# Kernel optimization log

Measured on AMD Instinct MI355X. Metric: run time of the kernel, lower is better.

## Reference

```python
import jax, jax.numpy as jnp
import numpy as np

D = 768      # hidden_dim
H = 12       # num_heads
DH = D // H  # head_dim = 64
L = 12       # num_layers
V = 50257    # vocab_size
M = 16       # mini_batch_size (TTT chunk)
LR = 1.0     # ttt_learning_rate
EPS = 1e-5
ROPE_BASE = 10000.0


def _ln(x, w, b):
    mu = jnp.mean(x, axis=-1, keepdims=True)
    var = jnp.mean((x - mu) ** 2, axis=-1, keepdims=True)
    return (x - mu) / jnp.sqrt(var + EPS) * w + b


def _rope(x):
    # x: (B, H, S, DH)
    S, dh = x.shape[2], x.shape[3]
    half = dh // 2
    freqs = 1.0 / (ROPE_BASE ** (jnp.arange(half, dtype=x.dtype) / half))
    ang = jnp.arange(S, dtype=x.dtype)[:, None] * freqs[None, :]  # (S, half)
    cos, sin = jnp.cos(ang), jnp.sin(ang)
    x1, x2 = x[..., :half], x[..., half:]
    return jnp.concatenate([x1 * cos - x2 * sin, x1 * sin + x2 * cos], axis=-1)


def setup_inputs() -> dict:
    key = jax.random.key(0)
    ks = jax.random.split(key, 12)
    std = 0.02
    B, S = 4, 1024
    inp = {
        "input_ids": jax.random.randint(ks[0], (B, S), 0, V),
        "tok_emb": jax.random.normal(ks[1], (V, D), jnp.float32) * std,
        "emb_ln_w": jnp.ones((D,), jnp.float32),
        "emb_ln_b": jnp.zeros((D,), jnp.float32),
        "wq": jax.random.normal(ks[2], (L, D, D), jnp.float32) * std,
        "wk": jax.random.normal(ks[3], (L, D, D), jnp.float32) * std,
        "wv": jax.random.normal(ks[4], (L, D, D), jnp.float32) * std,
        "wo": jax.random.normal(ks[5], (L, D, D), jnp.float32) * std,
        "n1w": jnp.ones((L, D), jnp.float32),
        "n1b": jnp.zeros((L, D), jnp.float32),
        "n2w": jnp.ones((L, D), jnp.float32),
        "n2b": jnp.zeros((L, D), jnp.float32),
        "m1w": jax.random.normal(ks[6], (L, D, 4 * D), jnp.float32) * std,
        "m1b": jnp.zeros((L, 4 * D), jnp.float32),
        "m2w": jax.random.normal(ks[7], (L, 4 * D, D), jnp.float32) * std,
        "m2b": jnp.zeros((L, D), jnp.float32),
        "onw": jnp.ones((D,), jnp.float32),
        "onb": jnp.zeros((D,), jnp.float32),
    }
    return inp


def _forward(input_ids, tok_emb, emb_ln_w, emb_ln_b, wq, wk, wv, wo,
             n1w, n1b, n2w, n2b, m1w, m1b, m2w, m2b, onw, onb):
    B, S = input_ids.shape
    nc = S // M
    eta = LR / M
    mask = jnp.tril(jnp.ones((M, M), tok_emb.dtype))

    x = tok_emb[input_ids]                      # (B, S, D) token embedding
    x = _ln(x, emb_ln_w, emb_ln_b)

    def layer(x, p):
        (lwq, lwk, lwv, lwo, ln1w, ln1b, ln2w, ln2b,
         lm1w, lm1b, lm2w, lm2b) = p
        h = _ln(x, ln1w, ln1b)

        def proj(w):
            return (h @ w).reshape(B, S, H, DH).transpose(0, 2, 1, 3)  # (B,H,S,DH)

        q, k, v = proj(lwq), proj(lwk), proj(lwv)
        q, k = _rope(q), _rope(k)

        def chunks(t):  # (B,H,S,DH) -> (nc,B,H,M,DH)
            return t.reshape(B, H, nc, M, DH).transpose(2, 0, 1, 3, 4)

        qc, kc, vc = chunks(q), chunks(k), chunks(v)
        W0 = jnp.zeros((B, H, DH, DH), x.dtype)  # fast-weight state per head

        def step(W, c):
            qm, km, vm = c                                   # (B,H,M,DH)
            # reconstruction error of current fast weights on this chunk
            E = jnp.einsum('bhmd,bhde->bhme', km, W) - vm    # (B,H,M,DH)
            # causal intra-chunk correction (dual form of per-token GD)
            A = jnp.einsum('bhmd,bhnd->bhmn', qm, km) * mask
            O = (jnp.einsum('bhmd,bhde->bhme', qm, W)
                 - eta * jnp.einsum('bhmn,bhne->bhme', A, E))
            Wn = W - eta * jnp.einsum('bhmd,bhme->bhde', km, E)
            return Wn, O

        _, O = jax.lax.scan(step, W0, (qc, kc, vc))          # (nc,B,H,M,DH)
        o = O.transpose(1, 2, 0, 3, 4).reshape(B, H, S, DH)
        o = o.transpose(0, 2, 1, 3).reshape(B, S, D)
        x = x + o @ lwo

        h2 = _ln(x, ln2w, ln2b)
        x = x + jax.nn.gelu(h2 @ lm1w + lm1b) @ lm2w + lm2b
        return x, None

    x, _ = jax.lax.scan(layer, x,
                        (wq, wk, wv, wo, n1w, n1b, n2w, n2b,
                         m1w, m1b, m2w, m2b))
    x = _ln(x, onw, onb)
    logits = x @ tok_emb.T                                    # tied LM head
    return logits


def reference(input_ids, tok_emb, emb_ln_w, emb_ln_b, wq, wk, wv, wo,
              n1w, n1b, n2w, n2b, m1w, m1b, m2w, m2b, onw, onb):
    return _forward(input_ids, tok_emb, emb_ln_w, emb_ln_b, wq, wk, wv, wo,
                    n1w, n1b, n2w, n2b, m1w, m1b, m2w, m2b, onw, onb)
```

## Files before the change

### kernel.cpp

```cpp
#include <hip/hip_runtime.h>
#include <cstdint>
#include <cstddef>

#define Dm 768
#define Hh 12
#define DHd 64
#define Ll 12
#define Vv 50257
#define Vp 50304
#define Tt 4096
#define Ff 3072
#define QS 2304
#define ETA (1.0f/16.0f)

typedef __attribute__((ext_vector_type(8))) _Float16 half8;
typedef __attribute__((ext_vector_type(8))) unsigned short ushort8;
typedef __attribute__((ext_vector_type(4))) float f32x4;

static __device__ __forceinline__ unsigned short f2h(float f){
  union { _Float16 h; unsigned short u; } c; c.h = (_Float16)f; return c.u;
}
static __device__ __forceinline__ float h2f(unsigned short u){
  union { unsigned short u; _Float16 h; } c; c.u = u; return (float)c.h;
}
static __device__ __forceinline__ float4 h4(ushort4 u){
  float4 f; f.x=h2f(u.x); f.y=h2f(u.y); f.z=h2f(u.z); f.w=h2f(u.w); return f;
}
static __device__ __forceinline__ void gload16(const void* g, void* l){
  __builtin_amdgcn_global_load_lds((const __attribute__((address_space(1))) unsigned int*)g,
                                   (__attribute__((address_space(3))) unsigned int*)l, 16, 0, 0);
}
static __device__ __forceinline__ size_t pan_off(int ks, size_t M, int row, int k){
  return ((size_t)ks*M + row)*128 + (size_t)(((k*2) ^ ((row & 7) << 4)));
}

__global__ __launch_bounds__(256)
void convwt_kernel(const float* __restrict__ src, unsigned short* __restrict__ dst,
                   int K, int Ns, int Nd, int coff)
{
  const int l  = blockIdx.y;
  const int nb = blockIdx.x % (Ns/64);
  const int ks = blockIdx.x / (Ns/64);
  const int t  = threadIdx.x;
  __shared__ float tile[64][65];
  const float* W = src + (size_t)l*K*Ns;
  {
    const int r = t >> 2, c0 = (t & 3) * 16;
    const float* s = W + (size_t)(ks*64 + r)*Ns + nb*64 + c0;
    #pragma unroll
    for (int i = 0; i < 4; ++i) {
      const float4 f = *(const float4*)(s + i*4);
      tile[r][c0+i*4+0]=f.x; tile[r][c0+i*4+1]=f.y; tile[r][c0+i*4+2]=f.z; tile[r][c0+i*4+3]=f.w;
    }
  }
  __syncthreads();
  const int n   = t >> 2;
  const int kk0 = (t & 3) * 16;
  const int gn  = coff + nb*64 + n;
  unsigned short bh[16];
  #pragma unroll
  for (int i = 0; i < 16; ++i) bh[i] = f2h(tile[kk0 + i][n]);
  const size_t rowb = ((size_t)l*K*Nd + ((size_t)ks*Nd + gn)*64) * 2;
  const int swz = (gn & 7) << 4;
  char* bD = (char*)dst + rowb;
  *(ushort8*)(bD + ((kk0*2)      ^ swz)) = *(ushort8*)&bh[0];
  *(ushort8*)(bD + ((kk0*2 + 16) ^ swz)) = *(ushort8*)&bh[8];
}

__global__ __launch_bounds__(256)
void convtok_kernel(const float* __restrict__ src, unsigned short* __restrict__ dst)
{
  const int total = 12 * Vp * 8;
  for (int gi = blockIdx.x*256 + threadIdx.x; gi < total; gi += gridDim.x*256) {
    const int j  = gi & 7;
    const int v  = (gi >> 3) % Vp;
    const int ks = gi / (8 * Vp);
    ushort8 u;
    if (v < Vv) {
      const float* s = src + (size_t)v*Dm + ks*64 + j*8;
      const float4 f0 = *(const float4*)s, f1 = *(const float4*)(s+4);
      u[0]=f2h(f0.x); u[1]=f2h(f0.y); u[2]=f2h(f0.z); u[3]=f2h(f0.w);
      u[4]=f2h(f1.x); u[5]=f2h(f1.y); u[6]=f2h(f1.z); u[7]=f2h(f1.w);
    } else {
      #pragma unroll
      for (int q = 0; q < 8; ++q) u[q] = 0;
    }
    const size_t rowb = ((size_t)ks*Vp + v) * 128;
    *(ushort8*)((char*)dst + rowb + ((j*16) ^ ((v&7)<<4))) = u;
  }
}

__global__ __launch_bounds__(256)
void rtab_kernel(float* __restrict__ rt)
{
  const int idx = blockIdx.x*256 + threadIdx.x;
  if (idx >= 1024*64) return;
  const int s = idx >> 6, c = idx & 63, d = c & 31;
  const float freq = powf(10000.0f, -(float)d * (1.0f/32.0f));
  const float ang  = (float)s * freq;
  rt[idx] = (c < 32) ? cosf(ang) : sinf(ang);
}

template<int OMODE>
__global__ __launch_bounds__(256)
void ln_kernel(const float* __restrict__ in, const int* __restrict__ ids,
               const float* __restrict__ w, const float* __restrict__ b,
               void* __restrict__ o1)
{
  const int row = blockIdx.x;
  const int t = threadIdx.x;
  const float* px = in + (ids ? (size_t)ids[row] * Dm : (size_t)row * Dm);
  float x0 = px[t], x1 = px[t+256], x2 = px[t+512];
  float s  = x0 + x1 + x2;
  float s2 = x0*x0 + x1*x1 + x2*x2;
  #pragma unroll
  for (int o = 32; o > 0; o >>= 1) { s += __shfl_xor(s, o); s2 += __shfl_xor(s2, o); }
  __shared__ float ls[4], ls2[4];
  if ((t & 63) == 0) { ls[t>>6] = s; ls2[t>>6] = s2; }
  __syncthreads();
  s  = ls[0]+ls[1]+ls[2]+ls[3];
  s2 = ls2[0]+ls2[1]+ls2[2]+ls2[3];
  const float mu  = s * (1.0f/Dm);
  const float var = s2 * (1.0f/Dm) - mu*mu;
  const float rs  = rsqrtf(var + 1e-5f);
  #pragma unroll
  for (int i = 0; i < 3; ++i) {
    const int c = t + i*256;
    const float xv = (i==0) ? x0 : (i==1) ? x1 : x2;
    const float vv_ = (xv-mu)*rs*w[c] + b[c];
    if (OMODE == 0) {
      ((float*)o1)[(size_t)row * Dm + c] = vv_;
    } else {
      *(unsigned short*)((char*)o1 + pan_off(c >> 6, Tt, row, c & 63)) = f2h(vv_);
    }
  }
}

static __device__ __forceinline__ float4 rot4(float4 a, float4 p, float4 rc, float4 rs, bool hi){
  float4 o;
  if (hi) { o.x = p.x*rs.x + a.x*rc.x; o.y = p.y*rs.y + a.y*rc.y;
            o.z = p.z*rs.z + a.z*rc.z; o.w = p.w*rs.w + a.w*rc.w; }
  else    { o.x = a.x*rc.x - p.x*rs.x; o.y = a.y*rc.y - p.y*rs.y;
            o.z = a.z*rc.z - p.z*rs.z; o.w = a.w*rc.w - p.w*rs.w; }
  return o;
}

__global__ __launch_bounds__(256)
void ttt_scan_kernel(const unsigned short* __restrict__ qkv, const float* __restrict__ rt,
                     unsigned short* __restrict__ ob)
{
  const int head = blockIdx.x >> 2;
  const int es   = blockIdx.x & 3;
  const int b  = head / Hh;
  const int hd = head % Hh;
  const int t  = threadIdx.x;
  __shared__ float Wm[16][68];
  __shared__ float kms[16][68];
  __shared__ float qms[16][68];
  __shared__ float EsT[16][20];
  __shared__ float Asc[16][20];

  const int e   = t & 15;
  const int m16 = t >> 4;
  const int sr  = t >> 4;
  const int sc  = (t & 15) * 4;
  const bool hi = (sc >= 32);

  for (int i = t; i < 16*68; i += 256) ((float*)Wm)[i] = 0.0f;

  const int tb0 = b * 1024;
  const size_t gbase = (size_t)hd * DHd;

  float4 krR, qrR;
  {
    const size_t ro = (size_t)(tb0 + sr)*QS + gbase;
    const float4 kr = h4(*(const ushort4*)&qkv[ro + Dm + sc]);
    const float4 kp = h4(*(const ushort4*)&qkv[ro + Dm + (sc^32)]);
    const float4 qr = h4(*(const ushort4*)&qkv[ro + sc]);
    const float4 qp = h4(*(const ushort4*)&qkv[ro + (sc^32)]);
    const float4 rc = *(const float4*)&rt[sr*64 + (sc&31)];
    const float4 rs = *(const float4*)&rt[sr*64 + 32 + (sc&31)];
    krR = rot4(kr, kp, rc, rs, hi);
    qrR = rot4(qr, qp, rc, rs, hi);
  }
  __syncthreads();

  for (int c = 0; c < 64; ++c) {
    const int tb = tb0 + c*16;
    *(float4*)&kms[sr][sc] = krR;
    *(float4*)&qms[sr][sc] = qrR;
    __syncthreads();
    if (c < 63) {
      const size_t ro = (size_t)(tb + 16 + sr)*QS + gbase;
      const float4 kr = h4(*(const ushort4*)&qkv[ro + Dm + sc]);
      const float4 kp = h4(*(const ushort4*)&qkv[ro + Dm + (sc^32)]);
      const float4 qr = h4(*(const ushort4*)&qkv[ro + sc]);
      const float4 qp = h4(*(const ushort4*)&qkv[ro + (sc^32)]);
      const int sN = (c+1)*16 + sr;
      const float4 rc = *(const float4*)&rt[sN*64 + (sc&31)];
      const float4 rs = *(const float4*)&rt[sN*64 + 32 + (sc&31)];
      krR = rot4(kr, kp, rc, rs, hi);
      qrR = rot4(qr, qp, rc, rs, hi);
    }
    const float vreg = h2f(qkv[(size_t)(tb+m16)*QS + 2*Dm + gbase + es*16 + e]);
    float aE = -vreg, aO = 0.0f, aA = 0.0f;
    #pragma unroll
    for (int d4 = 0; d4 < 64; d4 += 4) {
      const float4 wv = *(const float4*)&Wm[e][d4];
      const float4 km = *(const float4*)&kms[m16][d4];
      const float4 qm = *(const float4*)&qms[m16][d4];
      const float4 ke = *(const float4*)&kms[e][d4];
      aE += km.x*wv.x + km.y*wv.y + km.z*wv.z + km.w*wv.w;
      aO += qm.x*wv.x + qm.y*wv.y + qm.z*wv.z + qm.w*wv.w;
      aA += qm.x*ke.x + qm.y*ke.y + qm.z*ke.z + qm.w*ke.w;
    }
    EsT[e][m16] = aE;
    Asc[m16][e] = (e <= m16) ? (-ETA * aA) : 0.0f;
    __syncthreads();
    float esr[16];
    float acc = aO;
    #pragma unroll
    for (int n4 = 0; n4 < 16; n4 += 4) {
      const float4 ev = *(const float4*)&EsT[e][n4];
      const float4 av = *(const float4*)&Asc[m16][n4];
      esr[n4]=ev.x; esr[n4+1]=ev.y; esr[n4+2]=ev.z; esr[n4+3]=ev.w;
      acc += av.x*ev.x + av.y*ev.y + av.z*ev.z + av.w*ev.w;
    }
    *(unsigned short*)((char*)ob + pan_off(hd, Tt, tb + m16, es*16 + e)) = f2h(acc);
    {
      const int d0 = m16 * 4;
      float4 wacc; wacc.x = 0.0f; wacc.y = 0.0f; wacc.z = 0.0f; wacc.w = 0.0f;
      #pragma unroll
      for (int m = 0; m < 16; ++m) {
        const float4 km = *(const float4*)&kms[m][d0];
        const float ev = esr[m];
        wacc.x += km.x*ev; wacc.y += km.y*ev; wacc.z += km.z*ev; wacc.w += km.w*ev;
      }
      float4 wv = *(float4*)&Wm[e][d0];
      wv.x -= ETA*wacc.x; wv.y -= ETA*wacc.y; wv.z -= ETA*wacc.z; wv.w -= ETA*wacc.w;
      *(float4*)&Wm[e][d0] = wv;
    }
    __syncthreads();
  }
}

static __device__ __forceinline__ float gelu_f(float x){
  const float u = 0.7978845608028654f * (x + 0.044715f * x*x*x);
  return 0.5f * x * (1.0f + tanhf(u));
}

template<int TM, int TN, bool BIAS, bool GELU_, bool RES, int OUT>
__global__ __launch_bounds__(256)
void gemm_kernel(const unsigned short* __restrict__ A, const unsigned short* __restrict__ B,
                 const float* __restrict__ bias, const float* __restrict__ res,
                 void* __restrict__ o1, int M, int N, int K)
{
  constexpr int FM = TM / 32;
  constexpr int FN = TN / 32;
  __shared__ __attribute__((aligned(16))) unsigned short As[TM*64];
  __shared__ __attribute__((aligned(16))) unsigned short Bs[TN*64];
  const int t    = threadIdx.x;
  const int lane = t & 63;
  const int fr   = lane & 15;
  const int fg   = lane >> 4;
  const int wave = t >> 6;
  const int wm   = (wave >> 1) * (TM/2);
  const int wn   = (wave & 1) * (TN/2);
  const int row0 = blockIdx.y * TM;
  const int n0   = blockIdx.x * TN;

  f32x4 acc[FM][FN];
  #pragma unroll
  for (int i = 0; i < FM; ++i)
    #pragma unroll
    for (int j = 0; j < FN; ++j)
      #pragma unroll
      for (int r = 0; r < 4; ++r) acc[i][j][r] = 0.0f;

  for (int ks = 0; ks*64 < K; ++ks) {
    {
      const char* gB = (const char*)B + ((size_t)ks*N + n0) * 128;
      #pragma unroll
      for (int r = 0; r < TN/32; ++r) {
        const int chunk = (r*4 + wave) * 1024;
        gload16(gB + chunk + lane*16, (char*)Bs + chunk);
      }
    }
    {
      const char* gA = (const char*)A + ((size_t)ks*M + row0) * 128;
      #pragma unroll
      for (int r = 0; r < TM/32; ++r) {
        const int chunk = (r*4 + wave) * 1024;
        gload16(gA + chunk + lane*16, (char*)As + chunk);
      }
    }
    __syncthreads();
    #pragma unroll
    for (int kh = 0; kh < 2; ++kh) {
      half8 af[FM], bf[FN];
      const int swz = (fr & 7) << 4;
      #pragma unroll
      for (int mt = 0; mt < FM; ++mt)
        af[mt] = *(const half8*)((const char*)As + (((wm + mt*16 + fr)*128 + kh*64 + fg*16) ^ swz));
      #pragma unroll
      for (int nt = 0; nt < FN; ++nt)
        bf[nt] = *(const half8*)((const char*)Bs + (((wn + nt*16 + fr)*128 + kh*64 + fg*16) ^ swz));
      #pragma unroll
      for (int mt = 0; mt < FM; ++mt)
        #pragma unroll
        for (int nt = 0; nt < FN; ++nt)
          acc[mt][nt] = __builtin_amdgcn_mfma_f32_16x16x32_f16(af[mt], bf[nt], acc[mt][nt], 0, 0, 0);
    }
    __syncthreads();
  }

  #pragma unroll
  for (int mt = 0; mt < FM; ++mt) {
    #pragma unroll
    for (int nt = 0; nt < FN; ++nt) {
      const int col = n0 + wn + nt*16 + fr;
      const int rbase = row0 + wm + mt*16 + fg*4;
      const float bcol = BIAS ? bias[col] : 0.0f;
      #pragma unroll
      for (int r = 0; r < 4; ++r) {
        float val = acc[mt][nt][r];
        if (BIAS)  val += bcol;
        if (GELU_) val = gelu_f(val);
        if (OUT == 1) {
          *(unsigned short*)((char*)o1 + pan_off(col >> 6, M, rbase + r, col & 63)) = f2h(val);
        } else if (OUT == 2) {
          ((unsigned short*)o1)[(size_t)(rbase + r) * N + col] = f2h(val);
        } else {
          const size_t off = (size_t)(rbase + r) * N + col;
          float v2 = val;
          if (RES) v2 += res[off];
          ((float*)o1)[off] = v2;
        }
      }
    }
  }
}

template<bool PRE>
__global__ __launch_bounds__(256)
void logits_kernel(const unsigned short* __restrict__ hop, const float* __restrict__ tok,
                   const unsigned short* __restrict__ tokb, float* __restrict__ C)
{
  __shared__ __attribute__((aligned(16))) unsigned short As[128*64];
  __shared__ __attribute__((aligned(16))) unsigned short Bs[128*64];
  int bid = blockIdx.x;
  bid = (bid & 7) * 1572 + (bid >> 3);
  const int n0   = (bid >> 5) * 128;
  const int row0 = (bid & 31) * 128;

  const int t    = threadIdx.x;
  const int lane = t & 63;
  const int fr   = lane & 15;
  const int fg   = lane >> 4;
  const int wave = t >> 6;
  const int wm   = (wave >> 1) * 64;
  const int wn   = (wave & 1) * 64;
  const int arow = t >> 1;
  const int ach  = (t & 1) * 32;

  f32x4 acc[4][4];
  #pragma unroll
  for (int i = 0; i < 4; ++i)
    #pragma unroll
    for (int j = 0; j < 4; ++j)
      #pragma unroll
      for (int r = 0; r < 4; ++r) acc[i][j][r] = 0.0f;

  for (int ks = 0; ks < 12; ++ks) {
    {
      const char* gA = (const char*)hop + ((size_t)ks*Tt + row0) * 128;
      #pragma unroll
      for (int p = 0; p < 4; ++p) {
        const int off = p*4096 + t*16;
        const ushort8 u = *(const ushort8*)(gA + off);
        *(ushort8*)((char*)As + off) = u;
      }
    }
    if (PRE) {
      const char* gB = (const char*)tokb + ((size_t)ks*Vp + n0) * 128;
      #pragma unroll
      for (int p = 0; p < 4; ++p) {
        const int off = p*4096 + t*16;
        const ushort8 u = *(const ushort8*)(gB + off);
        *(ushort8*)((char*)Bs + off) = u;
      }
    } else {
      const int brow = n0 + arow;
      if (brow < Vv) {
        const float* src = &tok[(size_t)brow * Dm + ks*64 + ach];
        #pragma unroll
        for (int i = 0; i < 4; ++i) {
          const float4 f0 = *(const float4*)(src + i*8);
          const float4 f1 = *(const float4*)(src + i*8 + 4);
          ushort8 u;
          u[0]=f2h(f0.x); u[1]=f2h(f0.y); u[2]=f2h(f0.z); u[3]=f2h(f0.w);
          u[4]=f2h(f1.x); u[5]=f2h(f1.y); u[6]=f2h(f1.z); u[7]=f2h(f1.w);
          const int byt = (arow*128 + (ach + i*8)*2) ^ ((arow & 7) << 4);
          *(ushort8*)((char*)Bs + byt) = u;
        }
      } else {
        ushort8 z;
        #pragma unroll
        for (int j = 0; j < 8; ++j) z[j] = 0;
        #pragma unroll
        for (int i = 0; i < 4; ++i) {
          const int byt = (arow*128 + (ach + i*8)*2) ^ ((arow & 7) << 4);
          *(ushort8*)((char*)Bs + byt) = z;
        }
      }
    }
    __syncthreads();
    #pragma unroll
    for (int kh = 0; kh < 2; ++kh) {
      half8 af[4], bf[4];
      const int swz = (fr & 7) << 4;
      #pragma unroll
      for (int mt = 0; mt < 4; ++mt)
        af[mt] = *(const half8*)((const char*)As + (((wm + mt*16 + fr)*128 + kh*64 + fg*16) ^ swz));
      #pragma unroll
      for (int nt = 0; nt < 4; ++nt)
        bf[nt] = *(const half8*)((const char*)Bs + (((wn + nt*16 + fr)*128 + kh*64 + fg*16) ^ swz));
      #pragma unroll
      for (int mt = 0; mt < 4; ++mt)
        #pragma unroll
        for (int nt = 0; nt < 4; ++nt)
          acc[mt][nt] = __builtin_amdgcn_mfma_f32_16x16x32_f16(af[mt], bf[nt], acc[mt][nt], 0, 0, 0);
    }
    __syncthreads();
  }

  #pragma unroll
  for (int mt = 0; mt < 4; ++mt) {
    #pragma unroll
    for (int nt = 0; nt < 4; ++nt) {
      const int col = n0 + wn + nt*16 + fr;
      if (col < Vv) {
        const int rbase = row0 + wm + mt*16 + fg*4;
        #pragma unroll
        for (int r = 0; r < 4; ++r)
          C[(size_t)(rbase + r) * Vv + col] = acc[mt][nt][r];
      }
    }
  }
}

extern "C" void kernel_launch(void* const* d_in, const int* in_sizes, int n_in,
                              void* d_out, int out_size, void* d_ws, size_t ws_size,
                              hipStream_t stream)
{
  const int*   ids = (const int*)  d_in[0];
  const float* tok = (const float*)d_in[1];
  const float* ew  = (const float*)d_in[2];
  const float* eb  = (const float*)d_in[3];
  const float* wq  = (const float*)d_in[4];
  const float* wk  = (const float*)d_in[5];
  const float* wv  = (const float*)d_in[6];
  const float* wo  = (const float*)d_in[7];
  const float* n1w = (const float*)d_in[8];
  const float* n1b = (const float*)d_in[9];
  const float* n2w = (const float*)d_in[10];
  const float* n2b = (const float*)d_in[11];
  const float* m1w = (const float*)d_in[12];
  const float* m1b = (const float*)d_in[13];
  const float* m2w = (const float*)d_in[14];
  const float* m2b = (const float*)d_in[15];
  const float* onw = (const float*)d_in[16];
  const float* onb = (const float*)d_in[17];

  const size_t SP = (size_t)12 * Tt * 64;
  float* x = (float*)d_ws;
  unsigned short* hP = (unsigned short*)(x + (size_t)Tt * Dm);
  unsigned short* ho = hP + SP;
  float* rt = (float*)(ho + SP);
  unsigned short* tokb = (unsigned short*)(rt + 1024*64);
  const size_t ws_need = (size_t)Tt*Dm*4 + SP*2*2 + 1024*64*4 + (size_t)12*Vp*64*2;
  const bool pre = (ws_size >= ws_need);

  float* out = (float*)d_out;
  unsigned short* gP  = (unsigned short*)d_out;
  unsigned short* qkv = (unsigned short*)((char*)d_out + (size_t)28*1024*1024);
  unsigned short* obP = (unsigned short*)((char*)d_out + (size_t)50*1024*1024);
  unsigned short* wbase = (unsigned short*)((char*)d_out + (size_t)60*1024*1024);
  const size_t SQKV = (size_t)Ll * Dm * QS;
  const size_t SWO  = (size_t)Ll * Dm * Dm;
  const size_t SM   = (size_t)Ll * Dm * Ff;
  unsigned short* qkvW = wbase;
  unsigned short* woW  = qkvW + SQKV;
  unsigned short* m1W  = woW  + SWO;
  unsigned short* m2W  = m1W  + SM;

  convwt_kernel<<<dim3(12*12, Ll), 256, 0, stream>>>(wq, qkvW, Dm, Dm, QS, 0);
  convwt_kernel<<<dim3(12*12, Ll), 256, 0, stream>>>(wk, qkvW, Dm, Dm, QS, Dm);
  convwt_kernel<<<dim3(12*12, Ll), 256, 0, stream>>>(wv, qkvW, Dm, Dm, QS, 2*Dm);
  convwt_kernel<<<dim3(12*12, Ll), 256, 0, stream>>>(wo, woW, Dm, Dm, Dm, 0);
  convwt_kernel<<<dim3(12*48, Ll), 256, 0, stream>>>(m1w, m1W, Dm, Ff, Ff, 0);
  convwt_kernel<<<dim3(48*12, Ll), 256, 0, stream>>>(m2w, m2W, Ff, Dm, Dm, 0);
  rtab_kernel<<<256, 256, 0, stream>>>(rt);
  if (pre) convtok_kernel<<<2048, 256, 0, stream>>>(tok, tokb);

  ln_kernel<0><<<Tt, 256, 0, stream>>>(tok, ids, ew, eb, x);

  for (int l = 0; l < Ll; ++l) {
    ln_kernel<1><<<Tt, 256, 0, stream>>>(x, nullptr, n1w + l*Dm, n1b + l*Dm, hP);
    gemm_kernel<128,128,false,false,false,2><<<dim3(QS/128, Tt/128), 256, 0, stream>>>(
        hP, qkvW + (size_t)l*Dm*QS, nullptr, nullptr, qkv, Tt, QS, Dm);
    ttt_scan_kernel<<<192, 256, 0, stream>>>(qkv, rt, obP);
    gemm_kernel<128,64,false,false,true,0><<<dim3(Dm/64, Tt/128), 256, 0, stream>>>(
        obP, woW + (size_t)l*Dm*Dm, nullptr, x, x, Tt, Dm, Dm);
    ln_kernel<1><<<Tt, 256, 0, stream>>>(x, nullptr, n2w + l*Dm, n2b + l*Dm, hP);
    gemm_kernel<128,128,true,true,false,1><<<dim3(Ff/128, Tt/128), 256, 0, stream>>>(
        hP, m1W + (size_t)l*Dm*Ff, m1b + (size_t)l*Ff, nullptr, gP, Tt, Ff, Dm);
    gemm_kernel<128,64,true,false,true,0><<<dim3(Dm/64, Tt/128), 256, 0, stream>>>(
        gP, m2W + (size_t)l*Ff*Dm, m2b + (size_t)l*Dm, x, x, Tt, Dm, Ff);
  }

  ln_kernel<1><<<Tt, 256, 0, stream>>>(x, nullptr, onw, onb, ho);
  if (pre)
    logits_kernel<true><<<dim3(12576, 1), 256, 0, stream>>>(ho, tok, tokb, out);
  else
    logits_kernel<false><<<dim3(12576, 1), 256, 0, stream>>>(ho, tok, nullptr, out);
}
```

Measured before the change: 4.372 ms.

## Replace LDS-staged GEMM tiles with direct global-to-register MFMA fragment loads

New measurement: 4.923 ms. 1.13x slower.

```diff
diff --git a/kernel.cpp b/kernel.cpp
--- a/kernel.cpp
+++ b/kernel.cpp
@@ -25,10 +25,6 @@
 }
 static __device__ __forceinline__ float4 h4(ushort4 u){
   float4 f; f.x=h2f(u.x); f.y=h2f(u.y); f.z=h2f(u.z); f.w=h2f(u.w); return f;
-}
-static __device__ __forceinline__ void gload16(const void* g, void* l){
-  __builtin_amdgcn_global_load_lds((const __attribute__((address_space(1))) unsigned int*)g,
-                                   (__attribute__((address_space(3))) unsigned int*)l, 16, 0, 0);
 }
 static __device__ __forceinline__ size_t pan_off(int ks, size_t M, int row, int k){
   return ((size_t)ks*M + row)*128 + (size_t)(((k*2) ^ ((row & 7) << 4)));
@@ -249,25 +245,22 @@
   return 0.5f * x * (1.0f + tanhf(u));
 }
 
-template<int TM, int TN, bool BIAS, bool GELU_, bool RES, int OUT>
-__global__ __launch_bounds__(256)
-void gemm_kernel(const unsigned short* __restrict__ A, const unsigned short* __restrict__ B,
-                 const float* __restrict__ bias, const float* __restrict__ res,
-                 void* __restrict__ o1, int M, int N, int K)
-{
-  constexpr int FM = TM / 32;
-  constexpr int FN = TN / 32;
-  __shared__ __attribute__((aligned(16))) unsigned short As[TM*64];
-  __shared__ __attribute__((aligned(16))) unsigned short Bs[TN*64];
+template<int WTM, int WTN, bool BIAS, bool GELU_, bool RES, int OUT>
+__global__ __launch_bounds__(256)
+void gemm_nl(const unsigned short* __restrict__ A, const unsigned short* __restrict__ B,
+             const float* __restrict__ bias, const float* __restrict__ res,
+             void* __restrict__ o1, int M, int N, int K)
+{
+  constexpr int FM = WTM / 16;
+  constexpr int FN = WTN / 16;
   const int t    = threadIdx.x;
   const int lane = t & 63;
   const int fr   = lane & 15;
   const int fg   = lane >> 4;
-  const int wave = t >> 6;
-  const int wm   = (wave >> 1) * (TM/2);
-  const int wn   = (wave & 1) * (TN/2);
-  const int row0 = blockIdx.y * TM;
-  const int n0   = blockIdx.x * TN;
+  const int w    = t >> 6;
+  const int row0 = blockIdx.y * (2*WTM) + (w >> 1) * WTM;
+  const int n0   = blockIdx.x * (2*WTN) + (w & 1) * WTN;
+  const int swz  = (fr & 7) << 4;
 
   f32x4 acc[FM][FN];
   #pragma unroll
@@ -277,49 +270,36 @@
       #pragma unroll
       for (int r = 0; r < 4; ++r) acc[i][j][r] = 0.0f;
 
-  for (int ks = 0; ks*64 < K; ++ks) {
-    {
-      const char* gB = (const char*)B + ((size_t)ks*N + n0) * 128;
-      #pragma unroll
-      for (int r = 0; r < TN/32; ++r) {
-        const int chunk = (r*4 + wave) * 1024;
-        gload16(gB + chunk + lane*16, (char*)Bs + chunk);
-      }
-    }
-    {
-      const char* gA = (const char*)A + ((size_t)ks*M + row0) * 128;
-      #pragma unroll
-      for (int r = 0; r < TM/32; ++r) {
-        const int chunk = (r*4 + wave) * 1024;
-        gload16(gA + chunk + lane*16, (char*)As + chunk);
-      }
-    }
-    __syncthreads();
-    #pragma unroll
-    for (int kh = 0; kh < 2; ++kh) {
-      half8 af[FM], bf[FN];
-      const int swz = (fr & 7) << 4;
-      #pragma unroll
-      for (int mt = 0; mt < FM; ++mt)
-        af[mt] = *(const half8*)((const char*)As + (((wm + mt*16 + fr)*128 + kh*64 + fg*16) ^ swz));
-      #pragma unroll
-      for (int nt = 0; nt < FN; ++nt)
-        bf[nt] = *(const half8*)((const char*)Bs + (((wn + nt*16 + fr)*128 + kh*64 + fg*16) ^ swz));
+  const int NK = K >> 6;
+  for (int ks = 0; ks < NK; ++ks) {
+    const char* Ak = (const char*)A + ((size_t)ks * M) * 128;
+    const char* Bk = (const char*)B + ((size_t)ks * N) * 128;
+    half8 af[FM][2], bf[FN][2];
+    #pragma unroll
+    for (int mt = 0; mt < FM; ++mt)
+      #pragma unroll
+      for (int kh = 0; kh < 2; ++kh)
+        af[mt][kh] = *(const half8*)(Ak + (size_t)(row0 + mt*16 + fr)*128 + ((kh*64 + fg*16) ^ swz));
+    #pragma unroll
+    for (int nt = 0; nt < FN; ++nt)
+      #pragma unroll
+      for (int kh = 0; kh < 2; ++kh)
+        bf[nt][kh] = *(const half8*)(Bk + (size_t)(n0 + nt*16 + fr)*128 + ((kh*64 + fg*16) ^ swz));
+    #pragma unroll
+    for (int kh = 0; kh < 2; ++kh)
       #pragma unroll
       for (int mt = 0; mt < FM; ++mt)
         #pragma unroll
         for (int nt = 0; nt < FN; ++nt)
-          acc[mt][nt] = __builtin_amdgcn_mfma_f32_16x16x32_f16(af[mt], bf[nt], acc[mt][nt], 0, 0, 0);
-    }
-    __syncthreads();
+          acc[mt][nt] = __builtin_amdgcn_mfma_f32_16x16x32_f16(af[mt][kh], bf[nt][kh], acc[mt][nt], 0, 0, 0);
   }
 
   #pragma unroll
   for (int mt = 0; mt < FM; ++mt) {
     #pragma unroll
     for (int nt = 0; nt < FN; ++nt) {
-      const int col = n0 + wn + nt*16 + fr;
-      const int rbase = row0 + wm + mt*16 + fg*4;
+      const int col = n0 + nt*16 + fr;
+      const int rbase = row0 + mt*16 + fg*4;
       const float bcol = BIAS ? bias[col] : 0.0f;
       #pragma unroll
       for (int r = 0; r < 4; ++r) {
@@ -343,25 +323,22 @@
 
 template<bool PRE>
 __global__ __launch_bounds__(256)
-void logits_kernel(const unsigned short* __restrict__ hop, const float* __restrict__ tok,
-                   const unsigned short* __restrict__ tokb, float* __restrict__ C)
-{
-  __shared__ __attribute__((aligned(16))) unsigned short As[128*64];
-  __shared__ __attribute__((aligned(16))) unsigned short Bs[128*64];
+void logits_nl(const unsigned short* __restrict__ hop, const float* __restrict__ tok,
+               const unsigned short* __restrict__ tokb, float* __restrict__ C)
+{
   int bid = blockIdx.x;
   bid = (bid & 7) * 1572 + (bid >> 3);
-  const int n0   = (bid >> 5) * 128;
-  const int row0 = (bid & 31) * 128;
+  const int gn0   = (bid >> 5) * 128;
+  const int grow0 = (bid & 31) * 128;
 
   const int t    = threadIdx.x;
   const int lane = t & 63;
   const int fr   = lane & 15;
   const int fg   = lane >> 4;
-  const int wave = t >> 6;
-  const int wm   = (wave >> 1) * 64;
-  const int wn   = (wave & 1) * 64;
-  const int arow = t >> 1;
-  const int ach  = (t & 1) * 32;
+  const int w    = t >> 6;
+  const int row0 = grow0 + (w >> 1) * 64;
+  const int n0   = gn0   + (w & 1) * 64;
+  const int swz  = (fr & 7) << 4;
 
   f32x4 acc[4][4];
   #pragma unroll
@@ -372,75 +349,56 @@
       for (int r = 0; r < 4; ++r) acc[i][j][r] = 0.0f;
 
   for (int ks = 0; ks < 12; ++ks) {
-    {
-      const char* gA = (const char*)hop + ((size_t)ks*Tt + row0) * 128;
-      #pragma unroll
-      for (int p = 0; p < 4; ++p) {
-        const int off = p*4096 + t*16;
-        const ushort8 u = *(const ushort8*)(gA + off);
-        *(ushort8*)((char*)As + off) = u;
-      }
-    }
+    const char* Ak = (const char*)hop + ((size_t)ks * Tt) * 128;
+    half8 af[4][2], bf[4][2];
+    #pragma unroll
+    for (int mt = 0; mt < 4; ++mt)
+      #pragma unroll
+      for (int kh = 0; kh < 2; ++kh)
+        af[mt][kh] = *(const half8*)(Ak + (size_t)(row0 + mt*16 + fr)*128 + ((kh*64 + fg*16) ^ swz));
     if (PRE) {
-      const char* gB = (const char*)tokb + ((size_t)ks*Vp + n0) * 128;
-      #pragma unroll
-      for (int p = 0; p < 4; ++p) {
-        const int off = p*4096 + t*16;
-        const ushort8 u = *(const ushort8*)(gB + off);
-        *(ushort8*)((char*)Bs + off) = u;
-      }
+      const char* Bk = (const char*)tokb + ((size_t)ks * Vp) * 128;
+      #pragma unroll
+      for (int nt = 0; nt < 4; ++nt)
+        #pragma unroll
+        for (int kh = 0; kh < 2; ++kh)
+          bf[nt][kh] = *(const half8*)(Bk + (size_t)(n0 + nt*16 + fr)*128 + ((kh*64 + fg*16) ^ swz));
     } else {
-      const int brow = n0 + arow;
-      if (brow < Vv) {
-        const float* src = &tok[(size_t)brow * Dm + ks*64 + ach];
+      #pragma unroll
+      for (int nt = 0; nt < 4; ++nt) {
+        const int v = n0 + nt*16 + fr;
         #pragma unroll
-        for (int i = 0; i < 4; ++i) {
-          const float4 f0 = *(const float4*)(src + i*8);
-          const float4 f1 = *(const float4*)(src + i*8 + 4);
-          ushort8 u;
-          u[0]=f2h(f0.x); u[1]=f2h(f0.y); u[2]=f2h(f0.z); u[3]=f2h(f0.w);
-          u[4]=f2h(f1.x); u[5]=f2h(f1.y); u[6]=f2h(f1.z); u[7]=f2h(f1.w);
-          const int byt = (arow*128 + (ach + i*8)*2) ^ ((arow & 7) << 4);
-          *(ushort8*)((char*)Bs + byt) = u;
-        }
-      } else {
-        ushort8 z;
-        #pragma unroll
-        for (int j = 0; j < 8; ++j) z[j] = 0;
-        #pragma unroll
-        for (int i = 0; i < 4; ++i) {
-          const int byt = (arow*128 + (ach + i*8)*2) ^ ((arow & 7) << 4);
-          *(ushort8*)((char*)Bs + byt) = z;
+        for (int kh = 0; kh < 2; ++kh) {
+          half8 u;
+          if (v < Vv) {
+            const float* s = &tok[(size_t)v*Dm + ks*64 + kh*32 + fg*8];
+            const float4 f0 = *(const float4*)s, f1 = *(const float4*)(s+4);
+            u[0]=(_Float16)f0.x; u[1]=(_Float16)f0.y; u[2]=(_Float16)f0.z; u[3]=(_Float16)f0.w;
+            u[4]=(_Float16)f1.x; u[5]=(_Float16)f1.y; u[6]=(_Float16)f1.z; u[7]=(_Float16)f1.w;
+          } else {
+            #pragma unroll
+            for (int q = 0; q < 8; ++q) u[q] = (_Float16)0.0f;
+          }
+          bf[nt][kh] = u;
         }
       }
     }
-    __syncthreads();
-    #pragma unroll
-    for (int kh = 0; kh < 2; ++kh) {
-      half8 af[4], bf[4];
-      const int swz = (fr & 7) << 4;
-      #pragma unroll
-      for (int mt = 0; mt < 4; ++mt)
-        af[mt] = *(const half8*)((const char*)As + (((wm + mt*16 + fr)*128 + kh*64 + fg*16) ^ swz));
-      #pragma unroll
-      for (int nt = 0; nt < 4; ++nt)
-        bf[nt] = *(const half8*)((const char*)Bs + (((wn + nt*16 + fr)*128 + kh*64 + fg*16) ^ swz));
+    #pragma unroll
+    for (int kh = 0; kh < 2; ++kh)
       #pragma unroll
       for (int mt = 0; mt < 4; ++mt)
         #pragma unroll
         for (int nt = 0; nt < 4; ++nt)
-          acc[mt][nt] = __builtin_amdgcn_mfma_f32_16x16x32_f16(af[mt], bf[nt], acc[mt][nt], 0, 0, 0);
-    }
-    __syncthreads();
+          acc[mt][nt] = __builtin_amdgcn_mfma_f32_16x16x32_f16(af[mt][kh], bf[nt][kh], acc[mt][nt], 0, 0, 0);
   }
 
   #pragma unroll
   for (int mt = 0; mt < 4; ++mt) {
     #pragma unroll
     for (int nt = 0; nt < 4; ++nt) {
-      const int col = n0 + wn + nt*16 + fr;
+      const int col = n0 + nt*16 + fr;
       if (col < Vv) {
-        const int rbase = row0 + wm + mt*16 + fg*4;
+        const int rbase = row0 + mt*16 + fg*4;
         #pragma unroll
         for (int r = 0; r < 4; ++r)
           C[(size_t)(rbase + r) * Vv + col] = acc[mt][nt][r];
@@ -507,21 +465,21 @@
 
   for (int l = 0; l < Ll; ++l) {
     ln_kernel<1><<<Tt, 256, 0, stream>>>(x, nullptr, n1w + l*Dm, n1b + l*Dm, hP);
-    gemm_kernel<128,128,false,false,false,2><<<dim3(QS/128, Tt/128), 256, 0, stream>>>(
+    gemm_nl<64,64,false,false,false,2><<<dim3(QS/128, Tt/128), 256, 0, stream>>>(
         hP, qkvW + (size_t)l*Dm*QS, nullptr, nullptr, qkv, Tt, QS, Dm);
     ttt_scan_kernel<<<192, 256, 0, stream>>>(qkv, rt, obP);
-    gemm_kernel<128,64,false,false,true,0><<<dim3(Dm/64, Tt/128), 256, 0, stream>>>(
+    gemm_nl<32,32,false,false,true,0><<<dim3(Dm/64, Tt/64), 256, 0, stream>>>(
         obP, woW + (size_t)l*Dm*Dm, nullptr, x, x, Tt, Dm, Dm);
     ln_kernel<1><<<Tt, 256, 0, stream>>>(x, nullptr, n2w + l*Dm, n2b + l*Dm, hP);
-    gemm_kernel<128,128,true,true,false,1><<<dim3(Ff/128, Tt/128), 256, 0, stream>>>(
+    gemm_nl<64,64,true,true,false,1><<<dim3(Ff/128, Tt/128), 256, 0, stream>>>(
         hP, m1W + (size_t)l*Dm*Ff, m1b + (size_t)l*Ff, nullptr, gP, Tt, Ff, Dm);
-    gemm_kernel<128,64,true,false,true,0><<<dim3(Dm/64, Tt/128), 256, 0, stream>>>(
+    gemm_nl<32,32,true,false,true,0><<<dim3(Dm/64, Tt/64), 256, 0, stream>>>(
         gP, m2W + (size_t)l*Ff*Dm, m2b + (size_t)l*Dm, x, x, Tt, Dm, Ff);
   }
 
   ln_kernel<1><<<Tt, 256, 0, stream>>>(x, nullptr, onw, onb, ho);
   if (pre)
-    logits_kernel<true><<<dim3(12576, 1), 256, 0, stream>>>(ho, tok, tokb, out);
+    logits_nl<true><<<dim3(12576, 1), 256, 0, stream>>>(ho, tok, tokb, out);
   else
-    logits_kernel<false><<<dim3(12576, 1), 256, 0, stream>>>(ho, tok, nullptr, out);
-}
+    logits_nl<false><<<dim3(12576, 1), 256, 0, stream>>>(ho, tok, nullptr, out);
+}
```
